# Kernel optimization log

Measured on AMD Instinct MI355X. Metric: run time of the kernel, lower is better.

## Reference

```python
import jax, jax.numpy as jnp
import numpy as np

N_ATOMS = 20000
N_EDGES = 320000
NC = 16
N_RBF = 8
LOMAX = 2
CUTOFF = 4.0

# TensorProductLayer(max_x_way=2, max_y_way=2, max_z_way=2) combination list
TP_COMBOS = [(xw, yw, zw) for xw in range(3) for yw in range(3)
             for zw in range(abs(yw - xw), min(2, xw + yw) + 1, 2)]


def _aggregate(x, y, xw, yw, zw):
    # Contract the last c Cartesian dims of x with the first c Cartesian dims of y.
    # x: [E, nc] + (3,)*xw ; y: [E, nc] + (3,)*yw -> [E, nc] + (3,)*zw
    c = (xw + yw - zw) // 2
    E, nc = x.shape[0], x.shape[1]
    xa = x.reshape(E, nc, 3 ** (xw - c), 3 ** c)
    yb = y.reshape(E, nc, 3 ** c, 3 ** (yw - c))
    out = jnp.einsum('enak,enkb->enab', xa, yb)
    return out.reshape((E, nc) + (3,) * zw)


def _channel_linear(t, W, b=None):
    # nn.Linear applied over the channel dim (dim 1) of [B, nc] + (3,)*l tensors
    out = jnp.einsum('ec...,oc->eo...', t, W)
    if b is not None:
        out = out + b.reshape((1, -1) + (1,) * (t.ndim - 2))
    return out


def _forward(edge_index, positions, feats0, feats1, feats2, bessel_w, rbf_w,
             rbf_b, lin1_w, lin1_b, lin2_w, lin2_b, act_w, act_b, n_atoms):
    idx_i = edge_index[0]
    idx_j = edge_index[1]
    # find_distances
    rij = positions[idx_j] - positions[idx_i]              # [E,3]
    dij = jnp.sqrt(jnp.sum(rij * rij, axis=-1))            # [E]
    uij = rij / dij[:, None]                               # unit vectors
    # RBF: trainable BesselRBF * PolynomialCutoff(p=6)
    d = dij[:, None]                                       # [E,1]
    radial = jnp.sqrt(2.0 / CUTOFF) * jnp.sin(bessel_w * d) / d   # [E,n_rbf]
    t = d / CUTOFF
    poly = 1.0 - 28.0 * t**6 + 48.0 * t**7 - 21.0 * t**8
    env = jnp.where(t < 1.0, poly, 0.0)
    rbf_ij = radial * env                                  # [E,n_rbf]
    E = dij.shape[0]
    # find_moment(l): outer powers of the unit vector
    moments = [jnp.ones((E,), dij.dtype), uij, uij[:, :, None] * uij[:, None, :]]
    feats = [feats0, feats1, feats2]
    # gather neighbor feats + tensor linear mixing (bias only for l=0)
    x = {}
    for l in range(LOMAX + 1):
        g = feats[l][idx_j]
        x[l] = _channel_linear(g, lin1_w[l], lin1_b if l == 0 else None)
    # radial filters times moments
    y = {}
    for l in range(LOMAX + 1):
        fn = rbf_ij @ rbf_w[l].T + rbf_b[l]                # [E,nc]
        fn = fn.reshape((E, NC) + (1,) * l)                # expand_to(fn, l+2)
        y[l] = jnp.expand_dims(moments[l], 1) * fn         # [E,nc]+(3,)*l
    # equivariant tensor product
    msgs = {}
    for xw, yw, zw in TP_COMBOS:
        m = _aggregate(x[xw], y[yw], xw, yw, zw)
        msgs[zw] = msgs[zw] + m if zw in msgs else m
    # scatter-add aggregation per receiving node
    node_msg = {l: jax.ops.segment_sum(msgs[l], idx_i, num_segments=n_atoms)
                for l in range(LOMAX + 1)}
    # message processing: TensorLinearMixing -> TensorActivation
    out = {}
    for l in range(LOMAX + 1):
        h = _channel_linear(node_msg[l], lin2_w[l], lin2_b if l == 0 else None)
        if l == 0:
            out[l] = jax.nn.silu(h)
        else:
            flat = h.reshape(h.shape[0], h.shape[1], -1)
            norm = act_w[l - 1] * jnp.sum(flat * flat, axis=2) + act_b[l - 1]
            factor = jax.nn.sigmoid(norm).reshape(norm.shape + (1,) * l)
            out[l] = factor * h
    # residual update of node feats
    return (feats0 + out[0], feats1 + out[1], feats2 + out[2])


def setup_inputs() -> dict:
    key = jax.random.key(0)
    ks = jax.random.split(key, 16)
    positions = jax.random.uniform(ks[0], (N_ATOMS, 3), jnp.float32) * 5.0
    idx_i = jax.random.randint(ks[1], (N_EDGES,), 0, N_ATOMS)
    off = jax.random.randint(ks[2], (N_EDGES,), 1, N_ATOMS)
    idx_j = (idx_i + off) % N_ATOMS                        # guarantees i != j
    edge_index = jnp.stack([idx_i, idx_j]).astype(jnp.int32)
    atomic_numbers = jax.random.randint(ks[3], (N_ATOMS,), 1, 100)
    feats0 = jax.random.normal(ks[4], (N_ATOMS, NC), jnp.float32)
    feats1 = jax.random.normal(ks[5], (N_ATOMS, NC, 3), jnp.float32) * 0.3
    feats2 = jax.random.normal(ks[6], (N_ATOMS, NC, 3, 3), jnp.float32) * 0.3
    bessel_w = jnp.arange(1, N_RBF + 1, dtype=jnp.float32) * jnp.pi / CUTOFF
    s_rbf = 1.0 / np.sqrt(N_RBF)
    s_nc = 1.0 / np.sqrt(NC)
    rbf_w = jax.random.normal(ks[7], (3, NC, N_RBF), jnp.float32) * s_rbf
    rbf_b = jax.random.normal(ks[8], (3, NC), jnp.float32) * s_rbf
    lin1_w = jax.random.normal(ks[9], (3, NC, NC), jnp.float32) * s_nc
    lin1_b = jax.random.normal(ks[10], (NC,), jnp.float32) * s_nc
    lin2_w = jax.random.normal(ks[11], (3, NC, NC), jnp.float32) * s_nc
    lin2_b = jax.random.normal(ks[12], (NC,), jnp.float32) * s_nc
    act_w = jnp.ones((2, NC), jnp.float32)
    act_b = jnp.zeros((2, NC), jnp.float32)
    return {
        'edge_index': edge_index, 'positions': positions,
        'atomic_numbers': atomic_numbers,
        'feats0': feats0, 'feats1': feats1, 'feats2': feats2,
        'bessel_w': bessel_w, 'rbf_w': rbf_w, 'rbf_b': rbf_b,
        'lin1_w': lin1_w, 'lin1_b': lin1_b, 'lin2_w': lin2_w,
        'lin2_b': lin2_b, 'act_w': act_w, 'act_b': act_b,
    }


def reference(edge_index, positions, atomic_numbers, feats0, feats1, feats2,
              bessel_w, rbf_w, rbf_b, lin1_w, lin1_b, lin2_w, lin2_b,
              act_w, act_b):
    n_atoms = atomic_numbers.shape[0]
    return _forward(edge_index, positions, feats0, feats1, feats2, bessel_w,
                    rbf_w, rbf_b, lin1_w, lin1_b, lin2_w, lin2_b, act_w,
                    act_b, n_atoms)
```

## Files before the change

### kernel.cpp

```cpp
#include <hip/hip_runtime.h>
#include <math.h>

#define N_ATOMS 20000
#define N_EDGES 320000
#define NC 16
#define N_RBF 8
#define CUTOFF 4.0f
#define CAP 40

__device__ __forceinline__ unsigned bf16pair(float a, float b) {
    unsigned ua = __float_as_uint(a);
    ua = (ua + 0x7FFFu + ((ua >> 16) & 1u)) >> 16;
    unsigned ub = __float_as_uint(b);
    ub = (ub + 0x7FFFu + ((ub >> 16) & 1u)) >> 16;
    return ua | (ub << 16);
}
__device__ __forceinline__ float bflo(unsigned w) { return __uint_as_float(w << 16); }
__device__ __forceinline__ float bfhi(unsigned w) { return __uint_as_float(w & 0xFFFF0000u); }


__global__ __launch_bounds__(256) void pre_kernel(
    const int* __restrict__ idx_i, const int* __restrict__ idx_j,
    const float* __restrict__ pos, const float* __restrict__ f0,
    const float* __restrict__ f1, const float* __restrict__ f2,
    const float* __restrict__ w1, const float* __restrict__ b1,
    const float* __restrict__ bessel_w,
    int* __restrict__ cnt, float4* __restrict__ eslot, uint4* __restrict__ xgb) {
    __shared__ float4 sh[832];
    int tid = threadIdx.x;
    int b = blockIdx.x;
    if (b < 1250) {
        int a0 = b * 16;
        const float4* F0 = (const float4*)(f0 + a0 * 16);
        const float4* F1 = (const float4*)(f1 + a0 * 48);
        const float4* F2 = (const float4*)(f2 + a0 * 144);
        if (tid < 64) sh[tid] = F0[tid];
        if (tid < 192) sh[64 + tid] = F1[tid];
        sh[256 + tid] = F2[tid];
        sh[512 + tid] = F2[256 + tid];
        if (tid < 64) sh[768 + tid] = F2[512 + tid];
        __syncthreads();

        int al = tid >> 4;
        int o = tid & 15;
        int a = a0 + al;

        float w10[NC], w11[NC], w12[NC];
#pragma unroll
        for (int c = 0; c < NC; c++) {
            w10[c] = w1[0 * 256 + o * 16 + c];
            w11[c] = w1[1 * 256 + o * 16 + c];
            w12[c] = w1[2 * 256 + o * 16 + c];
        }
        const float4* G0 = sh + al * 4;
        const float4* G1 = sh + 64 + al * 12;
        const float4* G2 = sh + 256 + al * 36;
        float x0 = b1[o];
#pragma unroll
        for (int v = 0; v < 4; v++) {
            float4 q = G0[v];
            const float* qf = (const float*)&q;
#pragma unroll
            for (int t = 0; t < 4; t++) x0 += w10[4 * v + t] * qf[t];
        }
        float v1[3] = {0.f, 0.f, 0.f};
#pragma unroll
        for (int v = 0; v < 12; v++) {
            float4 q = G1[v];
            const float* qf = (const float*)&q;
#pragma unroll
            for (int t = 0; t < 4; t++) {
                int p = 4 * v + t;
                v1[p % 3] += w11[p / 3] * qf[t];
            }
        }
        float M[9] = {0.f, 0.f, 0.f, 0.f, 0.f, 0.f, 0.f, 0.f, 0.f};
#pragma unroll
        for (int v = 0; v < 36; v++) {
            float4 q = G2[v];
            const float* qf = (const float*)&q;
#pragma unroll
            for (int t = 0; t < 4; t++) {
                int p = 4 * v + t;
                M[p % 9] += w12[p / 9] * qf[t];
            }
        }
        uint4 lo, hi;
        lo.x = bf16pair(x0, v1[0]);
        lo.y = bf16pair(v1[1], v1[2]);
        lo.z = bf16pair(M[0], M[1]);
        lo.w = bf16pair(M[2], M[3]);
        hi.x = bf16pair(M[4], M[5]);
        hi.y = bf16pair(M[6], M[7]);
        hi.z = bf16pair(M[8], 0.f);
        hi.w = 0u;
        size_t base = ((size_t)a * 16 + o) * 2;
        xgb[base] = lo;
        xgb[base + 1] = hi;
    } else {
        int e = (b - 1250) * 256 + tid;
        int i = idx_i[e];
        int j = idx_j[e];
        int p = atomicAdd(&cnt[i], 1);
        if (p < CAP) {
            float dx = pos[j * 3 + 0] - pos[i * 3 + 0];
            float dy = pos[j * 3 + 1] - pos[i * 3 + 1];
            float dz = pos[j * 3 + 2] - pos[i * 3 + 2];
            float d2 = dx * dx + dy * dy + dz * dz;
            float rs = __builtin_amdgcn_rsqf(d2);
            float d = d2 * rs;
            float ux = dx * rs, uy = dy * rs, uz = dz * rs;

            float t = d * (1.0f / CUTOFF);
            float t3 = t * t * t, t6 = t3 * t3;
            float poly = 1.0f + t6 * (-28.0f + t * (48.0f - 21.0f * t));
            float env = (t < 1.0f) ? poly : 0.0f;
            float pref = 0.70710678118654752f * rs * env;

            float sx, cx;
            __sincosf(bessel_w[0] * d, &sx, &cx);
            float tw = 2.0f * cx;
            float sp = 0.f, sc = sx;
            float r[N_RBF];
#pragma unroll
            for (int k = 0; k < N_RBF; k++) {
                r[k] = pref * sc;
                float nx = tw * sc - sp;
                sp = sc;
                sc = nx;
            }
            uint4 rp;
            rp.x = bf16pair(r[0], r[1]);
            rp.y = bf16pair(r[2], r[3]);
            rp.z = bf16pair(r[4], r[5]);
            rp.w = bf16pair(r[6], r[7]);
            size_t q = ((size_t)i * CAP + p) * 2;
            eslot[q] = make_float4(ux, uy, uz, __int_as_float(j));
            eslot[q + 1] = *(float4*)&rp;
        }
    }
}


__global__ __launch_bounds__(64) void main_kernel(
    const int* __restrict__ cnt, const float4* __restrict__ eslot,
    const uint4* __restrict__ xgb, const float* __restrict__ f0,
    const float* __restrict__ f1, const float* __restrict__ f2,
    const float* __restrict__ rbf_w, const float* __restrict__ rbf_b,
    const float* __restrict__ w2, const float* __restrict__ b2,
    const float* __restrict__ act_w, const float* __restrict__ act_b,
    float* __restrict__ out) {
    int lane = threadIdx.x;
    int s = lane >> 4;
    int o = lane & 15;
    int a = blockIdx.x;

    float rw0[N_RBF], rw1[N_RBF], rw2[N_RBF];
#pragma unroll
    for (int k = 0; k < N_RBF; k++) {
        rw0[k] = rbf_w[0 * 128 + o * 8 + k];
        rw1[k] = rbf_w[1 * 128 + o * 8 + k];
        rw2[k] = rbf_w[2 * 128 + o * 8 + k];
    }
    float rb0 = rbf_b[o], rb1 = rbf_b[16 + o], rb2 = rbf_b[32 + o];
    int deg = cnt[a];
    if (deg > CAP) deg = CAP;
    int base = a * CAP;

    float res0 = 0.f, res[3];
    if (s == 0) {
        res0 = f0[a * 16 + o];
#pragma unroll
        for (int k = 0; k < 3; k++) res[k] = f1[a * 48 + o * 3 + k];
    } else {
        int k0 = (s - 1) * 3;
#pragma unroll
        for (int k = 0; k < 3; k++) res[k] = f2[a * 144 + o * 9 + k0 + k];
    }

    float nm0 = 0.f;
    float nm1[3] = {0.f, 0.f, 0.f};
    float nm2[9] = {0.f, 0.f, 0.f, 0.f, 0.f, 0.f, 0.f, 0.f, 0.f};

    int p = s;
    bool act = p < deg;
    int pn = p + 4;
    bool actn = pn < deg;
    float4 Ea = make_float4(0, 0, 0, 0), Eb = Ea, Ean = Ea, Ebn = Ea;
    uint4 XA = make_uint4(0, 0, 0, 0), XB = XA;
    if (act) {
        size_t q = (size_t)(base + p) * 2;
        Ea = eslot[q];
        Eb = eslot[q + 1];
        size_t xb = ((size_t)__float_as_int(Ea.w) * 16 + o) * 2;
        XA = xgb[xb];
        XB = xgb[xb + 1];
    }
    if (actn) {
        size_t q = (size_t)(base + pn) * 2;
        Ean = eslot[q];
        Ebn = eslot[q + 1];
    }

    while (__any(act)) {
        int pnn = pn + 4;
        bool actnn = pnn < deg;
        float4 Eann = make_float4(0, 0, 0, 0), Ebnn = Eann;
        if (actnn) {
            size_t q = (size_t)(base + pnn) * 2;
            Eann = eslot[q];
            Ebnn = eslot[q + 1];
        }
        uint4 XAn = make_uint4(0, 0, 0, 0), XBn = XAn;
        if (actn) {
            size_t xb = ((size_t)__float_as_int(Ean.w) * 16 + o) * 2;
            XAn = xgb[xb];
            XBn = xgb[xb + 1];
        }
        if (act) {
            float ux = Ea.x, uy = Ea.y, uz = Ea.z;
            uint4 R = *(uint4*)&Eb;
            float fn0 = rb0, fn1 = rb1, fn2 = rb2;
            float rr[N_RBF] = {bflo(R.x), bfhi(R.x), bflo(R.y), bfhi(R.y),
                               bflo(R.z), bfhi(R.z), bflo(R.w), bfhi(R.w)};
#pragma unroll
            for (int k = 0; k < N_RBF; k++) {
                fn0 += rw0[k] * rr[k];
                fn1 += rw1[k] * rr[k];
                fn2 += rw2[k] * rr[k];
            }

            float x0 = bflo(XA.x);
            float v1x = bfhi(XA.x), v1y = bflo(XA.y), v1z = bfhi(XA.y);
            float M[9] = {bflo(XA.z), bfhi(XA.z), bflo(XA.w), bfhi(XA.w),
                          bflo(XB.x), bfhi(XB.x), bflo(XB.y), bfhi(XB.y),
                          bflo(XB.z)};

            float d1 = v1x * ux + v1y * uy + v1z * uz;
            float Wv[3];
            Wv[0] = M[0] * ux + M[1] * uy + M[2] * uz;
            Wv[1] = M[3] * ux + M[4] * uy + M[5] * uz;
            Wv[2] = M[6] * ux + M[7] * uy + M[8] * uz;
            float q2 = Wv[0] * ux + Wv[1] * uy + Wv[2] * uz;

            nm0 += fn0 * x0 + fn1 * d1 + fn2 * q2;
            float u[3] = {ux, uy, uz};
            float vv[3] = {v1x, v1y, v1z};
#pragma unroll
            for (int bb = 0; bb < 3; bb++)
                nm1[bb] += fn0 * vv[bb] + fn1 * (x0 * u[bb] + Wv[bb]) + fn2 * d1 * u[bb];
#pragma unroll
            for (int ai = 0; ai < 3; ai++) {
                float coef = fn1 * vv[ai] + fn2 * (x0 * u[ai] + Wv[ai]);
#pragma unroll
                for (int bb = 0; bb < 3; bb++)
                    nm2[ai * 3 + bb] += fn0 * M[ai * 3 + bb] + coef * u[bb];
            }
        }
        p = pn; act = actn;
        Ea = Ean; Eb = Ebn; XA = XAn; XB = XBn;
        pn = pnn; actn = actnn;
        Ean = Eann; Ebn = Ebnn;
    }

#pragma unroll
    for (int mask = 16; mask <= 32; mask <<= 1) {
        nm0 += __shfl_xor(nm0, mask, 64);
#pragma unroll
        for (int k = 0; k < 3; k++) nm1[k] += __shfl_xor(nm1[k], mask, 64);
#pragma unroll
        for (int k = 0; k < 9; k++) nm2[k] += __shfl_xor(nm2[k], mask, 64);
    }

    float W0[16], WR[16];
    {
        const float4* wr0 = (const float4*)(w2 + 0 * 256 + o * 16);
        const float* wsel = (s == 0) ? (w2 + 1 * 256 + o * 16) : (w2 + 2 * 256 + o * 16);
        const float4* wrs = (const float4*)wsel;
#pragma unroll
        for (int v = 0; v < 4; v++) {
            *(float4*)&W0[4 * v] = wr0[v];
            *(float4*)&WR[4 * v] = wrs[v];
        }
    }
    float src0, src1, src2;
    if (s == 0) { src0 = nm1[0]; src1 = nm1[1]; src2 = nm1[2]; }
    else if (s == 1) { src0 = nm2[0]; src1 = nm2[1]; src2 = nm2[2]; }
    else if (s == 2) { src0 = nm2[3]; src1 = nm2[4]; src2 = nm2[5]; }
    else { src0 = nm2[6]; src1 = nm2[7]; src2 = nm2[8]; }

    float h0 = b2[o];
    float h[3] = {0.f, 0.f, 0.f};
#pragma unroll
    for (int c = 0; c < 16; c++) {
        h0 += W0[c] * __shfl(nm0, c, 16);
        float t0 = __shfl(src0, c, 16);
        float t1 = __shfl(src1, c, 16);
        float t2 = __shfl(src2, c, 16);
        h[0] += WR[c] * t0;
        h[1] += WR[c] * t1;
        h[2] += WR[c] * t2;
    }

    float sq = h[0] * h[0] + h[1] * h[1] + h[2] * h[2];
    float ss1 = (s == 0) ? sq : 0.f;
    float ss2 = (s == 0) ? 0.f : sq;
    ss1 += __shfl_xor(ss1, 16, 64);
    ss1 += __shfl_xor(ss1, 32, 64);
    ss2 += __shfl_xor(ss2, 16, 64);
    ss2 += __shfl_xor(ss2, 32, 64);
    float n1 = act_w[o] * ss1 + act_b[o];
    float g1f = 1.0f / (1.0f + expf(-n1));
    float n2 = act_w[16 + o] * ss2 + act_b[16 + o];
    float g2f = 1.0f / (1.0f + expf(-n2));

    if (s == 0) {
        float sig0 = 1.0f / (1.0f + expf(-h0));
        out[a * 16 + o] = res0 + h0 * sig0;
        int base1 = N_ATOMS * NC + a * 48 + o * 3;
#pragma unroll
        for (int k = 0; k < 3; k++)
            out[base1 + k] = res[k] + g1f * h[k];
    } else {
        int k0 = (s - 1) * 3;
        int base2 = N_ATOMS * NC * 4 + a * 144 + o * 9 + k0;
#pragma unroll
        for (int t = 0; t < 3; t++)
            out[base2 + t] = res[t] + g2f * h[t];
    }
}

extern "C" void kernel_launch(void* const* d_in, const int* in_sizes, int n_in,
                              void* d_out, int out_size, void* d_ws, size_t ws_size,
                              hipStream_t stream) {
    const int* edge_index = (const int*)d_in[0];
    const int* idx_i = edge_index;
    const int* idx_j = edge_index + N_EDGES;
    const float* pos = (const float*)d_in[1];
    const float* f0 = (const float*)d_in[3];
    const float* f1 = (const float*)d_in[4];
    const float* f2 = (const float*)d_in[5];
    const float* bessel_w = (const float*)d_in[6];
    const float* rbf_w = (const float*)d_in[7];
    const float* rbf_b = (const float*)d_in[8];
    const float* w1 = (const float*)d_in[9];
    const float* b1 = (const float*)d_in[10];
    const float* w2 = (const float*)d_in[11];
    const float* b2 = (const float*)d_in[12];
    const float* aw = (const float*)d_in[13];
    const float* ab = (const float*)d_in[14];
    float* out = (float*)d_out;

    int* cnt = (int*)d_ws;
    float4* eslot = (float4*)(cnt + 20480);
    uint4* xgb = (uint4*)(eslot + (size_t)2 * N_ATOMS * CAP);

    hipMemsetAsync(cnt, 0, N_ATOMS * sizeof(int), stream);
    pre_kernel<<<2500, 256, 0, stream>>>(idx_i, idx_j, pos, f0, f1, f2, w1, b1,
                                         bessel_w, cnt, eslot, xgb);
    main_kernel<<<N_ATOMS, 64, 0, stream>>>(cnt, eslot, xgb, f0, f1, f2,
                                            rbf_w, rbf_b, w2, b2, aw, ab, out);
}
```

Measured before the change: 84.62 us.

## Fuse memset, pre and main kernels into one cooperative persistent kernel

Replaces the memset plus two kernel launches with a single cooperative kernel that zeroes counters, runs the atom-linear and edge-bucketing phases, then processes atoms with four wavefronts per block, using grid-wide syncs between phases. The aim is to remove launch overhead and the inter-kernel gaps. In exchange it adds grid.sync costs and a fixed persistent grid sized from occupancy, which may give less latency hiding than the original 20000 small blocks. The old three-launch path is kept as a fallback if the cooperative launch fails.

```diff
diff --git a/kernel.cpp b/kernel.cpp
--- a/kernel.cpp
+++ b/kernel.cpp
@@ -1,5 +1,8 @@
 #include <hip/hip_runtime.h>
+#include <hip/hip_cooperative_groups.h>
 #include <math.h>
+
+namespace cg = cooperative_groups;
 
 #define N_ATOMS 20000
 #define N_EDGES 320000
@@ -19,141 +22,136 @@
 __device__ __forceinline__ float bfhi(unsigned w) { return __uint_as_float(w & 0xFFFF0000u); }
 
 
-__global__ __launch_bounds__(256) void pre_kernel(
-    const int* __restrict__ idx_i, const int* __restrict__ idx_j,
-    const float* __restrict__ pos, const float* __restrict__ f0,
+__device__ __forceinline__ void dev_atom_lin1(
+    int vb, int tid, float4* sh, const float* __restrict__ f0,
     const float* __restrict__ f1, const float* __restrict__ f2,
     const float* __restrict__ w1, const float* __restrict__ b1,
-    const float* __restrict__ bessel_w,
-    int* __restrict__ cnt, float4* __restrict__ eslot, uint4* __restrict__ xgb) {
-    __shared__ float4 sh[832];
-    int tid = threadIdx.x;
-    int b = blockIdx.x;
-    if (b < 1250) {
-        int a0 = b * 16;
-        const float4* F0 = (const float4*)(f0 + a0 * 16);
-        const float4* F1 = (const float4*)(f1 + a0 * 48);
-        const float4* F2 = (const float4*)(f2 + a0 * 144);
-        if (tid < 64) sh[tid] = F0[tid];
-        if (tid < 192) sh[64 + tid] = F1[tid];
-        sh[256 + tid] = F2[tid];
-        sh[512 + tid] = F2[256 + tid];
-        if (tid < 64) sh[768 + tid] = F2[512 + tid];
-        __syncthreads();
-
-        int al = tid >> 4;
-        int o = tid & 15;
-        int a = a0 + al;
-
-        float w10[NC], w11[NC], w12[NC];
-#pragma unroll
-        for (int c = 0; c < NC; c++) {
-            w10[c] = w1[0 * 256 + o * 16 + c];
-            w11[c] = w1[1 * 256 + o * 16 + c];
-            w12[c] = w1[2 * 256 + o * 16 + c];
-        }
-        const float4* G0 = sh + al * 4;
-        const float4* G1 = sh + 64 + al * 12;
-        const float4* G2 = sh + 256 + al * 36;
-        float x0 = b1[o];
-#pragma unroll
-        for (int v = 0; v < 4; v++) {
-            float4 q = G0[v];
-            const float* qf = (const float*)&q;
-#pragma unroll
-            for (int t = 0; t < 4; t++) x0 += w10[4 * v + t] * qf[t];
-        }
-        float v1[3] = {0.f, 0.f, 0.f};
-#pragma unroll
-        for (int v = 0; v < 12; v++) {
-            float4 q = G1[v];
-            const float* qf = (const float*)&q;
-#pragma unroll
-            for (int t = 0; t < 4; t++) {
-                int p = 4 * v + t;
-                v1[p % 3] += w11[p / 3] * qf[t];
-            }
-        }
-        float M[9] = {0.f, 0.f, 0.f, 0.f, 0.f, 0.f, 0.f, 0.f, 0.f};
-#pragma unroll
-        for (int v = 0; v < 36; v++) {
-            float4 q = G2[v];
-            const float* qf = (const float*)&q;
-#pragma unroll
-            for (int t = 0; t < 4; t++) {
-                int p = 4 * v + t;
-                M[p % 9] += w12[p / 9] * qf[t];
-            }
-        }
-        uint4 lo, hi;
-        lo.x = bf16pair(x0, v1[0]);
-        lo.y = bf16pair(v1[1], v1[2]);
-        lo.z = bf16pair(M[0], M[1]);
-        lo.w = bf16pair(M[2], M[3]);
-        hi.x = bf16pair(M[4], M[5]);
-        hi.y = bf16pair(M[6], M[7]);
-        hi.z = bf16pair(M[8], 0.f);
-        hi.w = 0u;
-        size_t base = ((size_t)a * 16 + o) * 2;
-        xgb[base] = lo;
-        xgb[base + 1] = hi;
-    } else {
-        int e = (b - 1250) * 256 + tid;
-        int i = idx_i[e];
-        int j = idx_j[e];
-        int p = atomicAdd(&cnt[i], 1);
-        if (p < CAP) {
-            float dx = pos[j * 3 + 0] - pos[i * 3 + 0];
-            float dy = pos[j * 3 + 1] - pos[i * 3 + 1];
-            float dz = pos[j * 3 + 2] - pos[i * 3 + 2];
-            float d2 = dx * dx + dy * dy + dz * dz;
-            float rs = __builtin_amdgcn_rsqf(d2);
-            float d = d2 * rs;
-            float ux = dx * rs, uy = dy * rs, uz = dz * rs;
-
-            float t = d * (1.0f / CUTOFF);
-            float t3 = t * t * t, t6 = t3 * t3;
-            float poly = 1.0f + t6 * (-28.0f + t * (48.0f - 21.0f * t));
-            float env = (t < 1.0f) ? poly : 0.0f;
-            float pref = 0.70710678118654752f * rs * env;
-
-            float sx, cx;
-            __sincosf(bessel_w[0] * d, &sx, &cx);
-            float tw = 2.0f * cx;
-            float sp = 0.f, sc = sx;
-            float r[N_RBF];
-#pragma unroll
-            for (int k = 0; k < N_RBF; k++) {
-                r[k] = pref * sc;
-                float nx = tw * sc - sp;
-                sp = sc;
-                sc = nx;
-            }
-            uint4 rp;
-            rp.x = bf16pair(r[0], r[1]);
-            rp.y = bf16pair(r[2], r[3]);
-            rp.z = bf16pair(r[4], r[5]);
-            rp.w = bf16pair(r[6], r[7]);
-            size_t q = ((size_t)i * CAP + p) * 2;
-            eslot[q] = make_float4(ux, uy, uz, __int_as_float(j));
-            eslot[q + 1] = *(float4*)&rp;
-        }
-    }
-}
-
-
-__global__ __launch_bounds__(64) void main_kernel(
-    const int* __restrict__ cnt, const float4* __restrict__ eslot,
+    uint4* __restrict__ xgb) {
+    int a0 = vb * 16;
+    const float4* F0 = (const float4*)(f0 + a0 * 16);
+    const float4* F1 = (const float4*)(f1 + a0 * 48);
+    const float4* F2 = (const float4*)(f2 + a0 * 144);
+    if (tid < 64) sh[tid] = F0[tid];
+    if (tid < 192) sh[64 + tid] = F1[tid];
+    sh[256 + tid] = F2[tid];
+    sh[512 + tid] = F2[256 + tid];
+    if (tid < 64) sh[768 + tid] = F2[512 + tid];
+    __syncthreads();
+
+    int al = tid >> 4;
+    int o = tid & 15;
+    int a = a0 + al;
+
+    float w10[NC], w11[NC], w12[NC];
+#pragma unroll
+    for (int c = 0; c < NC; c++) {
+        w10[c] = w1[0 * 256 + o * 16 + c];
+        w11[c] = w1[1 * 256 + o * 16 + c];
+        w12[c] = w1[2 * 256 + o * 16 + c];
+    }
+    const float4* G0 = sh + al * 4;
+    const float4* G1 = sh + 64 + al * 12;
+    const float4* G2 = sh + 256 + al * 36;
+    float x0 = b1[o];
+#pragma unroll
+    for (int v = 0; v < 4; v++) {
+        float4 q = G0[v];
+        const float* qf = (const float*)&q;
+#pragma unroll
+        for (int t = 0; t < 4; t++) x0 += w10[4 * v + t] * qf[t];
+    }
+    float v1[3] = {0.f, 0.f, 0.f};
+#pragma unroll
+    for (int v = 0; v < 12; v++) {
+        float4 q = G1[v];
+        const float* qf = (const float*)&q;
+#pragma unroll
+        for (int t = 0; t < 4; t++) {
+            int p = 4 * v + t;
+            v1[p % 3] += w11[p / 3] * qf[t];
+        }
+    }
+    float M[9] = {0.f, 0.f, 0.f, 0.f, 0.f, 0.f, 0.f, 0.f, 0.f};
+#pragma unroll
+    for (int v = 0; v < 36; v++) {
+        float4 q = G2[v];
+        const float* qf = (const float*)&q;
+#pragma unroll
+        for (int t = 0; t < 4; t++) {
+            int p = 4 * v + t;
+            M[p % 9] += w12[p / 9] * qf[t];
+        }
+    }
+    uint4 lo, hi;
+    lo.x = bf16pair(x0, v1[0]);
+    lo.y = bf16pair(v1[1], v1[2]);
+    lo.z = bf16pair(M[0], M[1]);
+    lo.w = bf16pair(M[2], M[3]);
+    hi.x = bf16pair(M[4], M[5]);
+    hi.y = bf16pair(M[6], M[7]);
+    hi.z = bf16pair(M[8], 0.f);
+    hi.w = 0u;
+    size_t base = ((size_t)a * 16 + o) * 2;
+    xgb[base] = lo;
+    xgb[base + 1] = hi;
+    __syncthreads();
+}
+
+__device__ __forceinline__ void dev_edge_bucket(
+    int e, const int* __restrict__ idx_i, const int* __restrict__ idx_j,
+    const float* __restrict__ pos, const float* __restrict__ bessel_w,
+    int* __restrict__ cnt, float4* __restrict__ eslot) {
+    int i = idx_i[e];
+    int j = idx_j[e];
+    int p = atomicAdd(&cnt[i], 1);
+    if (p < CAP) {
+        float dx = pos[j * 3 + 0] - pos[i * 3 + 0];
+        float dy = pos[j * 3 + 1] - pos[i * 3 + 1];
+        float dz = pos[j * 3 + 2] - pos[i * 3 + 2];
+        float d2 = dx * dx + dy * dy + dz * dz;
+        float rs = __builtin_amdgcn_rsqf(d2);
+        float d = d2 * rs;
+        float ux = dx * rs, uy = dy * rs, uz = dz * rs;
+
+        float t = d * (1.0f / CUTOFF);
+        float t3 = t * t * t, t6 = t3 * t3;
+        float poly = 1.0f + t6 * (-28.0f + t * (48.0f - 21.0f * t));
+        float env = (t < 1.0f) ? poly : 0.0f;
+        float pref = 0.70710678118654752f * rs * env;
+
+        float sx, cx;
+        __sincosf(bessel_w[0] * d, &sx, &cx);
+        float tw = 2.0f * cx;
+        float sp = 0.f, sc = sx;
+        float r[N_RBF];
+#pragma unroll
+        for (int k = 0; k < N_RBF; k++) {
+            r[k] = pref * sc;
+            float nx = tw * sc - sp;
+            sp = sc;
+            sc = nx;
+        }
+        uint4 rp;
+        rp.x = bf16pair(r[0], r[1]);
+        rp.y = bf16pair(r[2], r[3]);
+        rp.z = bf16pair(r[4], r[5]);
+        rp.w = bf16pair(r[6], r[7]);
+        size_t q = ((size_t)i * CAP + p) * 2;
+        eslot[q] = make_float4(ux, uy, uz, __int_as_float(j));
+        eslot[q + 1] = *(float4*)&rp;
+    }
+}
+
+__device__ __forceinline__ void dev_main_atom(
+    int a, int lane, const int* __restrict__ cnt, const float4* __restrict__ eslot,
     const uint4* __restrict__ xgb, const float* __restrict__ f0,
     const float* __restrict__ f1, const float* __restrict__ f2,
     const float* __restrict__ rbf_w, const float* __restrict__ rbf_b,
     const float* __restrict__ w2, const float* __restrict__ b2,
     const float* __restrict__ act_w, const float* __restrict__ act_b,
     float* __restrict__ out) {
-    int lane = threadIdx.x;
     int s = lane >> 4;
     int o = lane & 15;
-    int a = blockIdx.x;
 
     float rw0[N_RBF], rw1[N_RBF], rw2[N_RBF];
 #pragma unroll
@@ -330,34 +328,119 @@
     }
 }
 
+
+struct Params {
+    const int* idx_i;
+    const int* idx_j;
+    const float* pos;
+    const float* f0;
+    const float* f1;
+    const float* f2;
+    const float* bessel_w;
+    const float* rbf_w;
+    const float* rbf_b;
+    const float* w1;
+    const float* b1;
+    const float* w2;
+    const float* b2;
+    const float* act_w;
+    const float* act_b;
+    int* cnt;
+    float4* eslot;
+    uint4* xgb;
+    float* out;
+};
+
+
+__global__ __launch_bounds__(256, 2) void fused_kernel(Params P) {
+    cg::grid_group grid = cg::this_grid();
+    __shared__ float4 sh[832];
+    int tid = threadIdx.x;
+    int bid = blockIdx.x;
+    int G = gridDim.x;
+
+    for (int idx = bid * 256 + tid; idx < 20480; idx += G * 256) P.cnt[idx] = 0;
+    __threadfence();
+    grid.sync();
+
+    for (int vb = bid; vb < 2500; vb += G) {
+        if (vb < 1250) {
+            dev_atom_lin1(vb, tid, sh, P.f0, P.f1, P.f2, P.w1, P.b1, P.xgb);
+        } else {
+            int e = (vb - 1250) * 256 + tid;
+            dev_edge_bucket(e, P.idx_i, P.idx_j, P.pos, P.bessel_w, P.cnt, P.eslot);
+        }
+    }
+    __threadfence();
+    grid.sync();
+
+    int lane = tid & 63;
+    int nw = G * 4;
+    for (int a = bid * 4 + (tid >> 6); a < N_ATOMS; a += nw)
+        dev_main_atom(a, lane, P.cnt, P.eslot, P.xgb, P.f0, P.f1, P.f2, P.rbf_w,
+                      P.rbf_b, P.w2, P.b2, P.act_w, P.act_b, P.out);
+}
+
+
+__global__ __launch_bounds__(256) void pre_kernel(Params P) {
+    __shared__ float4 sh[832];
+    int b = blockIdx.x;
+    if (b < 1250) {
+        dev_atom_lin1(b, threadIdx.x, sh, P.f0, P.f1, P.f2, P.w1, P.b1, P.xgb);
+    } else {
+        int e = (b - 1250) * 256 + threadIdx.x;
+        dev_edge_bucket(e, P.idx_i, P.idx_j, P.pos, P.bessel_w, P.cnt, P.eslot);
+    }
+}
+
+__global__ __launch_bounds__(64) void main_kernel(Params P) {
+    dev_main_atom(blockIdx.x, threadIdx.x, P.cnt, P.eslot, P.xgb, P.f0, P.f1,
+                  P.f2, P.rbf_w, P.rbf_b, P.w2, P.b2, P.act_w, P.act_b, P.out);
+}
+
 extern "C" void kernel_launch(void* const* d_in, const int* in_sizes, int n_in,
                               void* d_out, int out_size, void* d_ws, size_t ws_size,
                               hipStream_t stream) {
     const int* edge_index = (const int*)d_in[0];
-    const int* idx_i = edge_index;
-    const int* idx_j = edge_index + N_EDGES;
-    const float* pos = (const float*)d_in[1];
-    const float* f0 = (const float*)d_in[3];
-    const float* f1 = (const float*)d_in[4];
-    const float* f2 = (const float*)d_in[5];
-    const float* bessel_w = (const float*)d_in[6];
-    const float* rbf_w = (const float*)d_in[7];
-    const float* rbf_b = (const float*)d_in[8];
-    const float* w1 = (const float*)d_in[9];
-    const float* b1 = (const float*)d_in[10];
-    const float* w2 = (const float*)d_in[11];
-    const float* b2 = (const float*)d_in[12];
-    const float* aw = (const float*)d_in[13];
-    const float* ab = (const float*)d_in[14];
-    float* out = (float*)d_out;
+
+    Params P;
+    P.idx_i = edge_index;
+    P.idx_j = edge_index + N_EDGES;
+    P.pos = (const float*)d_in[1];
+    P.f0 = (const float*)d_in[3];
+    P.f1 = (const float*)d_in[4];
+    P.f2 = (const float*)d_in[5];
+    P.bessel_w = (const float*)d_in[6];
+    P.rbf_w = (const float*)d_in[7];
+    P.rbf_b = (const float*)d_in[8];
+    P.w1 = (const float*)d_in[9];
+    P.b1 = (const float*)d_in[10];
+    P.w2 = (const float*)d_in[11];
+    P.b2 = (const float*)d_in[12];
+    P.act_w = (const float*)d_in[13];
+    P.act_b = (const float*)d_in[14];
+    P.out = (float*)d_out;
 
     int* cnt = (int*)d_ws;
-    float4* eslot = (float4*)(cnt + 20480);
-    uint4* xgb = (uint4*)(eslot + (size_t)2 * N_ATOMS * CAP);
-
-    hipMemsetAsync(cnt, 0, N_ATOMS * sizeof(int), stream);
-    pre_kernel<<<2500, 256, 0, stream>>>(idx_i, idx_j, pos, f0, f1, f2, w1, b1,
-                                         bessel_w, cnt, eslot, xgb);
-    main_kernel<<<N_ATOMS, 64, 0, stream>>>(cnt, eslot, xgb, f0, f1, f2,
-                                            rbf_w, rbf_b, w2, b2, aw, ab, out);
-}
+    P.cnt = cnt;
+    P.eslot = (float4*)(cnt + 20480);
+    P.xgb = (uint4*)(P.eslot + (size_t)2 * N_ATOMS * CAP);
+
+    int maxBlk = 0;
+    hipError_t oe = hipOccupancyMaxActiveBlocksPerMultiprocessor(&maxBlk,
+                                                                 fused_kernel, 256, 0);
+    hipError_t le = hipErrorUnknown;
+    if (oe == hipSuccess && maxBlk > 0) {
+        int grid = maxBlk * 256;
+        if (grid > 2048) grid = 2048;
+        void* args[] = {&P};
+        le = hipLaunchCooperativeKernel((void*)fused_kernel, dim3(grid), dim3(256),
+                                        args, 0, stream);
+    }
+    if (le != hipSuccess) {
+        (void)hipGetLastError();
+        hipMemsetAsync(cnt, 0, N_ATOMS * sizeof(int), stream);
+        pre_kernel<<<2500, 256, 0, stream>>>(P);
+        main_kernel<<<N_ATOMS, 64, 0, stream>>>(P);
+    }
+}
```

Result: slower. 276.0 us (+226.2%).

## Process two atoms per wavefront with interleaved branchless gather pipelines

Applied to the files above, without the earlier changes.

Each 64-thread block now handles two atoms, running two independent software pipelines whose gather loads are issued together before either computes. This aims to raise memory-level parallelism and hide gather latency, and it halves the block count. Loads are now unconditional: the index is clamped and inactive edges are masked by multiplying the filters by zero. The cost is higher register pressure, and the shared loop runs until the higher-degree atom of the pair is finished.

```diff
diff --git a/kernel.cpp b/kernel.cpp
--- a/kernel.cpp
+++ b/kernel.cpp
@@ -142,6 +142,182 @@
 }
 
 
+struct Pipe {
+    int base, deg, pnn;
+    bool act, actn, tact;
+    float4 Ea, Eb, Ean, Ebn, tEa, tEb;
+    uint4 XA, XB, tXA, tXB;
+    float nm0;
+    float nm1[3];
+    float nm2[9];
+};
+
+__device__ __forceinline__ void pipe_init(Pipe& S, int a, int s, int o,
+                                          const int* __restrict__ cnt,
+                                          const float4* __restrict__ eslot,
+                                          const uint4* __restrict__ xgb) {
+    int deg = cnt[a];
+    deg = deg > CAP ? CAP : deg;
+    S.deg = deg;
+    S.base = a * CAP;
+    S.act = s < deg;
+    S.actn = (s + 4) < deg;
+    S.pnn = s + 8;
+    S.nm0 = 0.f;
+#pragma unroll
+    for (int k = 0; k < 3; k++) S.nm1[k] = 0.f;
+#pragma unroll
+    for (int k = 0; k < 9; k++) S.nm2[k] = 0.f;
+    size_t q0 = (size_t)(S.base + s) * 2;
+    S.Ea = eslot[q0];
+    S.Eb = eslot[q0 + 1];
+    int j = S.act ? __float_as_int(S.Ea.w) : 0;
+    size_t xb = ((size_t)j * 16 + o) * 2;
+    S.XA = xgb[xb];
+    S.XB = xgb[xb + 1];
+    size_t q1 = (size_t)(S.base + s + 4) * 2;
+    S.Ean = eslot[q1];
+    S.Ebn = eslot[q1 + 1];
+}
+
+__device__ __forceinline__ void pipe_issue(Pipe& S, int o,
+                                           const float4* __restrict__ eslot,
+                                           const uint4* __restrict__ xgb) {
+    int idx = S.pnn < CAP ? S.pnn : CAP - 1;
+    S.tact = S.pnn < S.deg;
+    size_t q = (size_t)(S.base + idx) * 2;
+    S.tEa = eslot[q];
+    S.tEb = eslot[q + 1];
+    int jn = S.actn ? __float_as_int(S.Ean.w) : 0;
+    size_t xb = ((size_t)jn * 16 + o) * 2;
+    S.tXA = xgb[xb];
+    S.tXB = xgb[xb + 1];
+}
+
+__device__ __forceinline__ void pipe_compute(Pipe& S, const float* rw0,
+                                             const float* rw1, const float* rw2,
+                                             float rb0, float rb1, float rb2) {
+    float m = S.act ? 1.0f : 0.0f;
+    float ux = S.Ea.x, uy = S.Ea.y, uz = S.Ea.z;
+    uint4 R = *(uint4*)&S.Eb;
+    float rr[N_RBF] = {bflo(R.x), bfhi(R.x), bflo(R.y), bfhi(R.y),
+                       bflo(R.z), bfhi(R.z), bflo(R.w), bfhi(R.w)};
+    float fn0 = rb0, fn1 = rb1, fn2 = rb2;
+#pragma unroll
+    for (int k = 0; k < N_RBF; k++) {
+        fn0 += rw0[k] * rr[k];
+        fn1 += rw1[k] * rr[k];
+        fn2 += rw2[k] * rr[k];
+    }
+    fn0 *= m;
+    fn1 *= m;
+    fn2 *= m;
+
+    float x0 = bflo(S.XA.x);
+    float v1x = bfhi(S.XA.x), v1y = bflo(S.XA.y), v1z = bfhi(S.XA.y);
+    float M[9] = {bflo(S.XA.z), bfhi(S.XA.z), bflo(S.XA.w), bfhi(S.XA.w),
+                  bflo(S.XB.x), bfhi(S.XB.x), bflo(S.XB.y), bfhi(S.XB.y),
+                  bflo(S.XB.z)};
+
+    float d1 = v1x * ux + v1y * uy + v1z * uz;
+    float Wv[3];
+    Wv[0] = M[0] * ux + M[1] * uy + M[2] * uz;
+    Wv[1] = M[3] * ux + M[4] * uy + M[5] * uz;
+    Wv[2] = M[6] * ux + M[7] * uy + M[8] * uz;
+    float q2 = Wv[0] * ux + Wv[1] * uy + Wv[2] * uz;
+
+    S.nm0 += fn0 * x0 + fn1 * d1 + fn2 * q2;
+    float u[3] = {ux, uy, uz};
+    float vv[3] = {v1x, v1y, v1z};
+#pragma unroll
+    for (int bb = 0; bb < 3; bb++)
+        S.nm1[bb] += fn0 * vv[bb] + fn1 * (x0 * u[bb] + Wv[bb]) + fn2 * d1 * u[bb];
+#pragma unroll
+    for (int ai = 0; ai < 3; ai++) {
+        float coef = fn1 * vv[ai] + fn2 * (x0 * u[ai] + Wv[ai]);
+#pragma unroll
+        for (int bb = 0; bb < 3; bb++)
+            S.nm2[ai * 3 + bb] += fn0 * M[ai * 3 + bb] + coef * u[bb];
+    }
+
+    S.Ea = S.Ean;
+    S.Eb = S.Ebn;
+    S.XA = S.tXA;
+    S.XB = S.tXB;
+    S.act = S.actn;
+    S.Ean = S.tEa;
+    S.Ebn = S.tEb;
+    S.actn = S.tact;
+    S.pnn += 4;
+}
+
+__device__ __forceinline__ void epilogue(
+    const Pipe& S, int a, int s, int o, const float* W0, const float* WR,
+    float b2o, float aw1, float ab1, float aw2, float ab2,
+    const float* __restrict__ f0, const float* __restrict__ f1,
+    const float* __restrict__ f2, float* __restrict__ out) {
+    float nm0 = S.nm0;
+    float nm1[3] = {S.nm1[0], S.nm1[1], S.nm1[2]};
+    float nm2[9];
+#pragma unroll
+    for (int k = 0; k < 9; k++) nm2[k] = S.nm2[k];
+
+#pragma unroll
+    for (int mask = 16; mask <= 32; mask <<= 1) {
+        nm0 += __shfl_xor(nm0, mask, 64);
+#pragma unroll
+        for (int k = 0; k < 3; k++) nm1[k] += __shfl_xor(nm1[k], mask, 64);
+#pragma unroll
+        for (int k = 0; k < 9; k++) nm2[k] += __shfl_xor(nm2[k], mask, 64);
+    }
+
+    float src0, src1, src2;
+    if (s == 0) { src0 = nm1[0]; src1 = nm1[1]; src2 = nm1[2]; }
+    else if (s == 1) { src0 = nm2[0]; src1 = nm2[1]; src2 = nm2[2]; }
+    else if (s == 2) { src0 = nm2[3]; src1 = nm2[4]; src2 = nm2[5]; }
+    else { src0 = nm2[6]; src1 = nm2[7]; src2 = nm2[8]; }
+
+    float h0 = b2o;
+    float h[3] = {0.f, 0.f, 0.f};
+#pragma unroll
+    for (int c = 0; c < 16; c++) {
+        h0 += W0[c] * __shfl(nm0, c, 16);
+        float t0 = __shfl(src0, c, 16);
+        float t1 = __shfl(src1, c, 16);
+        float t2 = __shfl(src2, c, 16);
+        h[0] += WR[c] * t0;
+        h[1] += WR[c] * t1;
+        h[2] += WR[c] * t2;
+    }
+
+    float sq = h[0] * h[0] + h[1] * h[1] + h[2] * h[2];
+    float ss1 = (s == 0) ? sq : 0.f;
+    float ss2 = (s == 0) ? 0.f : sq;
+    ss1 += __shfl_xor(ss1, 16, 64);
+    ss1 += __shfl_xor(ss1, 32, 64);
+    ss2 += __shfl_xor(ss2, 16, 64);
+    ss2 += __shfl_xor(ss2, 32, 64);
+    float n1 = aw1 * ss1 + ab1;
+    float g1f = 1.0f / (1.0f + expf(-n1));
+    float n2 = aw2 * ss2 + ab2;
+    float g2f = 1.0f / (1.0f + expf(-n2));
+
+    if (s == 0) {
+        float sig0 = 1.0f / (1.0f + expf(-h0));
+        out[a * 16 + o] = f0[a * 16 + o] + h0 * sig0;
+        int base1 = N_ATOMS * NC + a * 48 + o * 3;
+#pragma unroll
+        for (int k = 0; k < 3; k++)
+            out[base1 + k] = f1[a * 48 + o * 3 + k] + g1f * h[k];
+    } else {
+        int k0 = (s - 1) * 3;
+        int base2 = N_ATOMS * NC * 4 + a * 144 + o * 9 + k0;
+#pragma unroll
+        for (int t = 0; t < 3; t++)
+            out[base2 + t] = f2[a * 144 + o * 9 + k0 + t] + g2f * h[t];
+    }
+}
+
 __global__ __launch_bounds__(64) void main_kernel(
     const int* __restrict__ cnt, const float4* __restrict__ eslot,
     const uint4* __restrict__ xgb, const float* __restrict__ f0,
@@ -153,7 +329,8 @@
     int lane = threadIdx.x;
     int s = lane >> 4;
     int o = lane & 15;
-    int a = blockIdx.x;
+    int aA = blockIdx.x * 2;
+    int aB = aA + 1;
 
     float rw0[N_RBF], rw1[N_RBF], rw2[N_RBF];
 #pragma unroll
@@ -163,113 +340,16 @@
         rw2[k] = rbf_w[2 * 128 + o * 8 + k];
     }
     float rb0 = rbf_b[o], rb1 = rbf_b[16 + o], rb2 = rbf_b[32 + o];
-    int deg = cnt[a];
-    if (deg > CAP) deg = CAP;
-    int base = a * CAP;
-
-    float res0 = 0.f, res[3];
-    if (s == 0) {
-        res0 = f0[a * 16 + o];
-#pragma unroll
-        for (int k = 0; k < 3; k++) res[k] = f1[a * 48 + o * 3 + k];
-    } else {
-        int k0 = (s - 1) * 3;
-#pragma unroll
-        for (int k = 0; k < 3; k++) res[k] = f2[a * 144 + o * 9 + k0 + k];
-    }
-
-    float nm0 = 0.f;
-    float nm1[3] = {0.f, 0.f, 0.f};
-    float nm2[9] = {0.f, 0.f, 0.f, 0.f, 0.f, 0.f, 0.f, 0.f, 0.f};
-
-    int p = s;
-    bool act = p < deg;
-    int pn = p + 4;
-    bool actn = pn < deg;
-    float4 Ea = make_float4(0, 0, 0, 0), Eb = Ea, Ean = Ea, Ebn = Ea;
-    uint4 XA = make_uint4(0, 0, 0, 0), XB = XA;
-    if (act) {
-        size_t q = (size_t)(base + p) * 2;
-        Ea = eslot[q];
-        Eb = eslot[q + 1];
-        size_t xb = ((size_t)__float_as_int(Ea.w) * 16 + o) * 2;
-        XA = xgb[xb];
-        XB = xgb[xb + 1];
-    }
-    if (actn) {
-        size_t q = (size_t)(base + pn) * 2;
-        Ean = eslot[q];
-        Ebn = eslot[q + 1];
-    }
-
-    while (__any(act)) {
-        int pnn = pn + 4;
-        bool actnn = pnn < deg;
-        float4 Eann = make_float4(0, 0, 0, 0), Ebnn = Eann;
-        if (actnn) {
-            size_t q = (size_t)(base + pnn) * 2;
-            Eann = eslot[q];
-            Ebnn = eslot[q + 1];
-        }
-        uint4 XAn = make_uint4(0, 0, 0, 0), XBn = XAn;
-        if (actn) {
-            size_t xb = ((size_t)__float_as_int(Ean.w) * 16 + o) * 2;
-            XAn = xgb[xb];
-            XBn = xgb[xb + 1];
-        }
-        if (act) {
-            float ux = Ea.x, uy = Ea.y, uz = Ea.z;
-            uint4 R = *(uint4*)&Eb;
-            float fn0 = rb0, fn1 = rb1, fn2 = rb2;
-            float rr[N_RBF] = {bflo(R.x), bfhi(R.x), bflo(R.y), bfhi(R.y),
-                               bflo(R.z), bfhi(R.z), bflo(R.w), bfhi(R.w)};
-#pragma unroll
-            for (int k = 0; k < N_RBF; k++) {
-                fn0 += rw0[k] * rr[k];
-                fn1 += rw1[k] * rr[k];
-                fn2 += rw2[k] * rr[k];
-            }
-
-            float x0 = bflo(XA.x);
-            float v1x = bfhi(XA.x), v1y = bflo(XA.y), v1z = bfhi(XA.y);
-            float M[9] = {bflo(XA.z), bfhi(XA.z), bflo(XA.w), bfhi(XA.w),
-                          bflo(XB.x), bfhi(XB.x), bflo(XB.y), bfhi(XB.y),
-                          bflo(XB.z)};
-
-            float d1 = v1x * ux + v1y * uy + v1z * uz;
-            float Wv[3];
-            Wv[0] = M[0] * ux + M[1] * uy + M[2] * uz;
-            Wv[1] = M[3] * ux + M[4] * uy + M[5] * uz;
-            Wv[2] = M[6] * ux + M[7] * uy + M[8] * uz;
-            float q2 = Wv[0] * ux + Wv[1] * uy + Wv[2] * uz;
-
-            nm0 += fn0 * x0 + fn1 * d1 + fn2 * q2;
-            float u[3] = {ux, uy, uz};
-            float vv[3] = {v1x, v1y, v1z};
-#pragma unroll
-            for (int bb = 0; bb < 3; bb++)
-                nm1[bb] += fn0 * vv[bb] + fn1 * (x0 * u[bb] + Wv[bb]) + fn2 * d1 * u[bb];
-#pragma unroll
-            for (int ai = 0; ai < 3; ai++) {
-                float coef = fn1 * vv[ai] + fn2 * (x0 * u[ai] + Wv[ai]);
-#pragma unroll
-                for (int bb = 0; bb < 3; bb++)
-                    nm2[ai * 3 + bb] += fn0 * M[ai * 3 + bb] + coef * u[bb];
-            }
-        }
-        p = pn; act = actn;
-        Ea = Ean; Eb = Ebn; XA = XAn; XB = XBn;
-        pn = pnn; actn = actnn;
-        Ean = Eann; Ebn = Ebnn;
-    }
-
-#pragma unroll
-    for (int mask = 16; mask <= 32; mask <<= 1) {
-        nm0 += __shfl_xor(nm0, mask, 64);
-#pragma unroll
-        for (int k = 0; k < 3; k++) nm1[k] += __shfl_xor(nm1[k], mask, 64);
-#pragma unroll
-        for (int k = 0; k < 9; k++) nm2[k] += __shfl_xor(nm2[k], mask, 64);
+
+    Pipe A, B;
+    pipe_init(A, aA, s, o, cnt, eslot, xgb);
+    pipe_init(B, aB, s, o, cnt, eslot, xgb);
+
+    while (__any(A.act | B.act)) {
+        pipe_issue(A, o, eslot, xgb);
+        pipe_issue(B, o, eslot, xgb);
+        pipe_compute(A, rw0, rw1, rw2, rb0, rb1, rb2);
+        pipe_compute(B, rw0, rw1, rw2, rb0, rb1, rb2);
     }
 
     float W0[16], WR[16];
@@ -283,51 +363,12 @@
             *(float4*)&WR[4 * v] = wrs[v];
         }
     }
-    float src0, src1, src2;
-    if (s == 0) { src0 = nm1[0]; src1 = nm1[1]; src2 = nm1[2]; }
-    else if (s == 1) { src0 = nm2[0]; src1 = nm2[1]; src2 = nm2[2]; }
-    else if (s == 2) { src0 = nm2[3]; src1 = nm2[4]; src2 = nm2[5]; }
-    else { src0 = nm2[6]; src1 = nm2[7]; src2 = nm2[8]; }
-
-    float h0 = b2[o];
-    float h[3] = {0.f, 0.f, 0.f};
-#pragma unroll
-    for (int c = 0; c < 16; c++) {
-        h0 += W0[c] * __shfl(nm0, c, 16);
-        float t0 = __shfl(src0, c, 16);
-        float t1 = __shfl(src1, c, 16);
-        float t2 = __shfl(src2, c, 16);
-        h[0] += WR[c] * t0;
-        h[1] += WR[c] * t1;
-        h[2] += WR[c] * t2;
-    }
-
-    float sq = h[0] * h[0] + h[1] * h[1] + h[2] * h[2];
-    float ss1 = (s == 0) ? sq : 0.f;
-    float ss2 = (s == 0) ? 0.f : sq;
-    ss1 += __shfl_xor(ss1, 16, 64);
-    ss1 += __shfl_xor(ss1, 32, 64);
-    ss2 += __shfl_xor(ss2, 16, 64);
-    ss2 += __shfl_xor(ss2, 32, 64);
-    float n1 = act_w[o] * ss1 + act_b[o];
-    float g1f = 1.0f / (1.0f + expf(-n1));
-    float n2 = act_w[16 + o] * ss2 + act_b[16 + o];
-    float g2f = 1.0f / (1.0f + expf(-n2));
-
-    if (s == 0) {
-        float sig0 = 1.0f / (1.0f + expf(-h0));
-        out[a * 16 + o] = res0 + h0 * sig0;
-        int base1 = N_ATOMS * NC + a * 48 + o * 3;
-#pragma unroll
-        for (int k = 0; k < 3; k++)
-            out[base1 + k] = res[k] + g1f * h[k];
-    } else {
-        int k0 = (s - 1) * 3;
-        int base2 = N_ATOMS * NC * 4 + a * 144 + o * 9 + k0;
-#pragma unroll
-        for (int t = 0; t < 3; t++)
-            out[base2 + t] = res[t] + g2f * h[t];
-    }
+    float b2o = b2[o];
+    float aw1 = act_w[o], ab1 = act_b[o];
+    float aw2 = act_w[16 + o], ab2 = act_b[16 + o];
+
+    epilogue(A, aA, s, o, W0, WR, b2o, aw1, ab1, aw2, ab2, f0, f1, f2, out);
+    epilogue(B, aB, s, o, W0, WR, b2o, aw1, ab1, aw2, ab2, f0, f1, f2, out);
 }
 
 extern "C" void kernel_launch(void* const* d_in, const int* in_sizes, int n_in,
@@ -358,6 +399,6 @@
     hipMemsetAsync(cnt, 0, N_ATOMS * sizeof(int), stream);
     pre_kernel<<<2500, 256, 0, stream>>>(idx_i, idx_j, pos, f0, f1, f2, w1, b1,
                                          bessel_w, cnt, eslot, xgb);
-    main_kernel<<<N_ATOMS, 64, 0, stream>>>(cnt, eslot, xgb, f0, f1, f2,
-                                            rbf_w, rbf_b, w2, b2, aw, ab, out);
-}
+    main_kernel<<<N_ATOMS / 2, 64, 0, stream>>>(cnt, eslot, xgb, f0, f1, f2,
+                                                rbf_w, rbf_b, w2, b2, aw, ab, out);
+}
```

Measured after the change: 89.52 us. 1.06x slower.
